# Performance work log

Measured on AMD Instinct MI355X. Metric: run time of the kernel, lower is better.

## Reference

```python
import jax, jax.numpy as jnp
import numpy as np

B, N, V, H, R, A, IN, K = 64, 512, 64, 512, 4, 18, 128, 32
EPS = 1e-8


def setup_inputs() -> dict:
    key = jax.random.key(0)
    ks = jax.random.split(key, 20)
    g = lambda i, shape, s=1.0: jax.random.normal(ks[i], shape, jnp.float32) * s
    u = lambda i, shape: jax.random.uniform(ks[i], shape, dtype=jnp.float32)
    cin = IN + R * V
    return dict(
        x=g(0, (B, IN)),
        h=g(1, (B, H), 0.1),
        c=g(2, (B, H), 0.1),
        memory=g(3, (B, N, V), 0.1),
        read_weights=u(4, (B, R, N)),
        write_weights=u(5, (B, N)),
        usage=u(6, (B, N)),
        link_matrix=u(7, (B, N, N)) * 0.01,
        precedence_weights=u(8, (B, N)),
        W_ih=g(9, (4 * H, cin), 0.05), W_hh=g(10, (4 * H, H), 0.05),
        b_ih=jnp.zeros(4 * H, jnp.float32), b_hh=jnp.zeros(4 * H, jnp.float32),
        W_read=g(11, (R, V + 4, H), 0.05), b_read=jnp.zeros((R, V + 4), jnp.float32),
        W_write=g(12, (3 * V + 3, H), 0.05), b_write=jnp.zeros(3 * V + 3, jnp.float32),
        W_pol=g(13, (A, H), 0.05), b_pol=jnp.zeros(A, jnp.float32),
        W_val=g(14, (1, H), 0.05), b_val=jnp.zeros(1, jnp.float32),
    )


def reference(x, h, c, memory, read_weights, write_weights, usage, link_matrix,
              precedence_weights, W_ih, W_hh, b_ih, b_hh, W_read, b_read,
              W_write, b_write, W_pol, b_pol, W_val, b_val):
    # ---- read heads (vectorized over R) ----
    ro = jnp.einsum('roh,bh->bro', W_read, h) + b_read            # [B,R,V+4]
    rkey = ro[..., :V]
    rbeta = jax.nn.softplus(ro[..., V])                           # [B,R]
    rpi = jax.nn.softmax(ro[..., V + 1:V + 4], axis=-1)           # backward/content/forward gates
    mem_norm = jnp.maximum(jnp.linalg.norm(memory, axis=-1), EPS)  # [B,N]
    key_norm = jnp.maximum(jnp.linalg.norm(rkey, axis=-1), EPS)    # [B,R]
    sim = jnp.einsum('bnv,brv->brn', memory, rkey) / (mem_norm[:, None, :] * key_norm[..., None])
    scores = rbeta[..., None] * sim                                # [B,R,N]
    kth = jax.lax.top_k(scores, K)[0][..., -1:]                    # sparse top-k mask
    cw = jax.nn.softmax(jnp.where(scores >= kth, scores, -jnp.inf), axis=-1)
    fw = jnp.einsum('bnm,brm->brn', link_matrix, read_weights)     # forward weighting L w
    bw = jnp.einsum('bmn,brm->brn', link_matrix, read_weights)     # backward weighting L^T w
    w_r = rpi[..., 0:1] * bw + rpi[..., 1:2] * cw + rpi[..., 2:3] * fw  # [B,R,N]
    rvec = jnp.einsum('brn,bnv->brv', w_r, memory).reshape(B, R * V)
    # ---- LSTM controller (torch LSTMCell gate order i,f,g,o) ----
    gates = jnp.concatenate([x, rvec], -1) @ W_ih.T + h @ W_hh.T + b_ih + b_hh
    i_g, f_g, g_g, o_g = jnp.split(gates, 4, axis=-1)
    c_new = jax.nn.sigmoid(f_g) * c + jax.nn.sigmoid(i_g) * jnp.tanh(g_g)
    h_new = jax.nn.sigmoid(o_g) * jnp.tanh(c_new)
    # ---- write head ----
    wo = h_new @ W_write.T + b_write                               # [B,3V+3]
    wkey = wo[:, :V]
    erase = jax.nn.sigmoid(wo[:, V:2 * V])
    add = jnp.tanh(wo[:, 2 * V:3 * V])
    wbeta = jax.nn.softplus(wo[:, 3 * V])
    g_a = jax.nn.sigmoid(wo[:, 3 * V + 1])
    g_w = jax.nn.sigmoid(wo[:, 3 * V + 2])
    wkey_norm = jnp.maximum(jnp.linalg.norm(wkey, axis=-1), EPS)
    wsim = jnp.einsum('bnv,bv->bn', memory, wkey) / (mem_norm * wkey_norm[:, None])
    cw_w = jax.nn.softmax(wbeta[:, None] * wsim, axis=-1)
    # allocation weighting from sorted usage (DNC Eq. 1)
    idx = jnp.argsort(usage, axis=-1)
    u_sorted = jnp.take_along_axis(usage, idx, -1)
    prod_prev = jnp.concatenate([jnp.ones((B, 1), usage.dtype), jnp.cumprod(u_sorted, -1)[:, :-1]], -1)
    a_sorted = (1.0 - u_sorted) * prod_prev
    alloc = jnp.take_along_axis(a_sorted, jnp.argsort(idx, -1), -1)
    write_w = g_w[:, None] * (g_a[:, None] * alloc + (1.0 - g_a)[:, None] * cw_w)  # [B,N]
    # ---- memory erase/add ----
    mem_new = memory * (1.0 - write_w[:, :, None] * erase[:, None, :]) + write_w[:, :, None] * add[:, None, :]
    # ---- usage (psi detached as in torch.no_grad) ----
    psi = jax.lax.stop_gradient(jnp.prod(1.0 - w_r, axis=1))
    usage_new = (usage + write_weights - usage * write_weights) * psi
    # ---- link matrix + precedence ----
    ws = jnp.sum(write_w, -1, keepdims=True)
    prec_new = (1.0 - ws) * precedence_weights + write_w
    decay = (1.0 - write_w[:, :, None]) * (1.0 - write_w[:, None, :])
    link_new = decay * link_matrix + write_w[:, :, None] * precedence_weights[:, None, :]
    link_new = link_new * (1.0 - jnp.eye(N, dtype=link_new.dtype))
    # ---- actor/critic heads ----
    logits = h_new @ W_pol.T + b_pol
    value = h_new @ W_val.T + b_val
    return (logits, value, h_new, c_new, mem_new, w_r, write_w, usage_new, link_new, prec_new)
```

## Files before the change

kernel.cpp:

```cpp
#include <hip/hip_runtime.h>
#include <math.h>

constexpr int Bb = 64, Nn = 512, Vv = 64, Hh = 512, Rr = 4, Aa = 18, INp = 128, KTOP = 32;
constexpr int CIN = 384;
constexpr int WOUT = 195;
#define EPSf 1e-8f

__device__ __forceinline__ float sigmoidf(float x){ return 1.f/(1.f+expf(-x)); }
__device__ __forceinline__ float softplusf(float x){ return (x>20.f)? x : log1pf(expf(x)); }
__device__ __forceinline__ float wave_reduce(float v){
  #pragma unroll
  for(int o=32;o>0;o>>=1) v += __shfl_down(v, o, 64);
  return v;
}
__device__ __forceinline__ unsigned f2ord(float f){
  unsigned u = __float_as_uint(f);
  return (u & 0x80000000u) ? ~u : (u | 0x80000000u);
}
__device__ __forceinline__ const float* wrow_sel(int d, const float* Ww, const float* Wp, const float* Wv){
  return (d < WOUT) ? Ww + (size_t)d*Hh : ((d < WOUT+Aa) ? Wp + (size_t)(d-WOUT)*Hh : Wv);
}

__global__ void k_stage1(const float* __restrict__ link, const float* __restrict__ rw,
                         const float* __restrict__ Wr, const float* __restrict__ brd,
                         const float* __restrict__ h, const float* __restrict__ mem,
                         float* __restrict__ fw, float* __restrict__ bwpart,
                         float* __restrict__ rvec, float* __restrict__ rp,
                         float* __restrict__ cw) {
  __shared__ __align__(16) float smem[6208];
  if (blockIdx.x < 512) {
    float* lds   = smem;
    float* ldsrw = smem + 4160;
    int b  = blockIdx.x >> 3;
    int st = blockIdx.x & 7;
    int tid = threadIdx.x;
    {
      const float4* rw4 = (const float4*)(rw + b*Rr*Nn);
      float4* lrw4 = (float4*)ldsrw;
      lrw4[tid] = rw4[tid];
      lrw4[tid+256] = rw4[tid+256];
    }
    if (blockIdx.x < 64) rvec[blockIdx.x*256 + tid] = 0.f;
    __syncthreads();
    int row = tid & 63, rr = tid >> 6;
    float facc = 0.f;
    const float4* lb4 = (const float4*)(link + (size_t)b*Nn*Nn);
    const float* rwn = ldsrw + rr*512 + st*64;
    for (int jt = 0; jt < 8; ++jt) {
      #pragma unroll
      for (int q = 0; q < 4; ++q) {
        int idx4 = tid*4 + q;
        int tr = idx4 >> 4;
        int c4 = idx4 & 15;
        float4 v = lb4[(size_t)(st*64 + tr)*128 + jt*16 + c4];
        int base = tr*65 + c4*4;
        lds[base] = v.x; lds[base+1] = v.y; lds[base+2] = v.z; lds[base+3] = v.w;
      }
      __syncthreads();
      const float* rwj = ldsrw + rr*512 + jt*64;
      float a = 0.f;
      #pragma unroll 8
      for (int j = 0; j < 64; ++j) a += lds[row*65 + j] * rwj[j];
      facc += a;
      float bacc = 0.f;
      #pragma unroll 8
      for (int n = 0; n < 64; ++n) bacc += lds[n*65 + row] * rwn[n];
      bwpart[((size_t)(st*Bb + b)*Rr + rr)*Nn + jt*64 + row] = bacc;
      __syncthreads();
    }
    fw[(b*Rr + rr)*Nn + st*64 + row] = facc;
  } else {
    float* sh  = smem;
    float* sro = smem + 512;
    unsigned long long* sk = (unsigned long long*)(smem + 592);
    float* sred = smem + 1616;
    float* skv  = smem + 1620;
    int blk = blockIdx.x - 512;
    int b = blk >> 2, r = blk & 3;
    int tid = threadIdx.x;
    int wv = tid >> 6, lane = tid & 63;
    const float* hb = h + b*Hh;
    for (int i = tid; i < 512; i += 256) sh[i] = hb[i];
    __syncthreads();
    const float* wbase = Wr + (size_t)(r*68)*Hh;
    int pbase = wv*17;
    #pragma unroll
    for (int g = 0; g < 4; ++g) {
      int p = pbase + g*4;
      const float *w0 = wbase + (size_t)p*Hh, *w1 = w0 + Hh, *w2 = w1 + Hh, *w3 = w2 + Hh;
      float a0=0,a1=0,a2=0,a3=0;
      #pragma unroll
      for (int t = 0; t < 8; ++t) {
        int k = lane + 64*t; float hv = sh[k];
        a0 += w0[k]*hv; a1 += w1[k]*hv; a2 += w2[k]*hv; a3 += w3[k]*hv;
      }
      #pragma unroll
      for (int o = 32; o > 0; o >>= 1) {
        a0 += __shfl_down(a0,o,64); a1 += __shfl_down(a1,o,64);
        a2 += __shfl_down(a2,o,64); a3 += __shfl_down(a3,o,64);
      }
      if (lane == 0) {
        sro[p]   = a0 + brd[r*68+p];   sro[p+1] = a1 + brd[r*68+p+1];
        sro[p+2] = a2 + brd[r*68+p+2]; sro[p+3] = a3 + brd[r*68+p+3];
      }
    }
    {
      int p = pbase + 16;
      const float* w0 = wbase + (size_t)p*Hh;
      float a0 = 0.f;
      #pragma unroll
      for (int t = 0; t < 8; ++t) { int k = lane + 64*t; a0 += w0[k]*sh[k]; }
      a0 = wave_reduce(a0);
      if (lane == 0) sro[p] = a0 + brd[r*68+p];
    }
    __syncthreads();
    if (wv == 0) {
      float kv = sro[lane];
      float k2 = wave_reduce(kv*kv);
      if (lane == 0) {
        float rbeta = softplusf(sro[64]);
        float sc = rbeta / fmaxf(sqrtf(k2), EPSf);
        float e0 = sro[65], e1 = sro[66], e2 = sro[67];
        float mm = fmaxf(e0, fmaxf(e1, e2));
        float x0 = expf(e0-mm), x1 = expf(e1-mm), x2 = expf(e2-mm);
        float inv = 1.f/(x0+x1+x2);
        float* rpb = rp + (b*4 + r)*4;
        rpb[0] = sc; rpb[1] = x0*inv; rpb[2] = x1*inv; rpb[3] = x2*inv;
        sro[68] = sc;
      }
    }
    __syncthreads();
    float sc = sro[68];
    const float4* key4 = (const float4*)sro;
    float v0, v1;
    {
      const float4* m4 = (const float4*)(mem + ((size_t)(b*Nn + tid))*Vv);
      float dot=0.f, nrm=0.f;
      #pragma unroll
      for (int i = 0; i < 16; ++i) {
        float4 mv = m4[i]; float4 kk = key4[i];
        dot += mv.x*kk.x + mv.y*kk.y + mv.z*kk.z + mv.w*kk.w;
        nrm += mv.x*mv.x + mv.y*mv.y + mv.z*mv.z + mv.w*mv.w;
      }
      v0 = sc * dot / fmaxf(sqrtf(nrm), EPSf);
    }
    {
      const float4* m4 = (const float4*)(mem + ((size_t)(b*Nn + tid + 256))*Vv);
      float dot=0.f, nrm=0.f;
      #pragma unroll
      for (int i = 0; i < 16; ++i) {
        float4 mv = m4[i]; float4 kk = key4[i];
        dot += mv.x*kk.x + mv.y*kk.y + mv.z*kk.z + mv.w*kk.w;
        nrm += mv.x*mv.x + mv.y*mv.y + mv.z*mv.z + mv.w*mv.w;
      }
      v1 = sc * dot / fmaxf(sqrtf(nrm), EPSf);
    }
    unsigned long long k0 = ((unsigned long long)f2ord(v0) << 32) | (unsigned)(511 - tid);
    unsigned long long k1 = ((unsigned long long)f2ord(v1) << 32) | (unsigned)(255 - tid);
    sk[tid] = k0; sk[tid+256] = k1;
    __syncthreads();
    int c0 = 0, c1 = 0;
    #pragma unroll 8
    for (int j = 0; j < 512; ++j) {
      unsigned long long kj = sk[j];
      c0 += (kj > k0); c1 += (kj > k1);
    }
    if (c0 == KTOP-1) skv[0] = v0;
    if (c1 == KTOP-1) skv[0] = v1;
    if (c0 == 0) skv[1] = v0;
    if (c1 == 0) skv[1] = v1;
    __syncthreads();
    float kth = skv[0], mx = skv[1];
    float e0 = (v0 >= kth) ? expf(v0-mx) : 0.f;
    float e1 = (v1 >= kth) ? expf(v1-mx) : 0.f;
    float s = wave_reduce(e0+e1);
    if (lane == 0) sred[wv] = s;
    __syncthreads();
    float inv = 1.f/(sred[0]+sred[1]+sred[2]+sred[3]);
    int brr = b*4 + r;
    cw[brr*Nn+tid]     = e0*inv;
    cw[brr*Nn+tid+256] = e1*inv;
  }
}

__global__ void k_wrrv(const float* __restrict__ bwpart, const float* __restrict__ cw,
                       const float* __restrict__ fw, const float* __restrict__ rp,
                       const float* __restrict__ usage, const float* __restrict__ wwt,
                       const float* __restrict__ mem,
                       float* __restrict__ out_wr, float* __restrict__ out_usage,
                       float* __restrict__ rvec) {
  __shared__ float swr[4][64];
  int b = blockIdx.x >> 3, ch = blockIdx.x & 7;
  int tid = threadIdx.x;
  int r = tid >> 6, nl = tid & 63;
  int n = ch*64 + nl;
  int brr = b*4 + r;
  float bwv = 0.f;
  #pragma unroll
  for (int chh = 0; chh < 8; ++chh)
    bwv += bwpart[((size_t)(chh*Bb + b)*Rr + r)*Nn + n];
  const float* rpb = rp + brr*4;
  float w = rpb[1]*bwv + rpb[2]*cw[brr*Nn+n] + rpb[3]*fw[brr*Nn+n];
  out_wr[brr*Nn+n] = w;
  swr[r][nl] = w;
  __syncthreads();
  if (tid < 64) {
    int idx = b*Nn + ch*64 + tid;
    float psi = (1.f-swr[0][tid])*(1.f-swr[1][tid])*(1.f-swr[2][tid])*(1.f-swr[3][tid]);
    float u = usage[idx], wt = wwt[idx];
    out_usage[idx] = (u + wt - u*wt) * psi;
  }
  const float* mb = mem + ((size_t)b*Nn + ch*64)*Vv + nl;
  float acc = 0.f;
  #pragma unroll 16
  for (int t = 0; t < 64; ++t) acc += swr[r][t] * mb[t*Vv];
  atomicAdd(&rvec[brr*Vv + nl], acc);
}

__global__ void k_gates_lstm(const float* __restrict__ x, const float* __restrict__ rvec,
                             const float* __restrict__ h, const float* __restrict__ Wih,
                             const float* __restrict__ Whh, const float* __restrict__ bih,
                             const float* __restrict__ bhh, const float* __restrict__ c,
                             float* __restrict__ out_h, float* __restrict__ out_c) {
  int gid = blockIdx.x*4 + (threadIdx.x>>6);
  int lane = threadIdx.x & 63;
  int hh = gid >> 4;
  int bt = gid & 15;
  float acc[4][4] = {};
  #pragma unroll
  for (int t = 0; t < 6; ++t) {
    int k = lane + 64*t;
    float u[4], w[4];
    #pragma unroll
    for (int i = 0; i < 4; ++i) {
      int b = bt*4 + i;
      u[i] = (k < INp) ? x[b*INp + k] : rvec[b*(Rr*Vv) + k - INp];
      w[i] = Wih[(size_t)(i*Hh + hh)*CIN + k];
    }
    #pragma unroll
    for (int g = 0; g < 4; ++g)
      #pragma unroll
      for (int bb = 0; bb < 4; ++bb) acc[g][bb] += w[g]*u[bb];
  }
  #pragma unroll
  for (int t = 0; t < 8; ++t) {
    int k = lane + 64*t;
    float u[4], w[4];
    #pragma unroll
    for (int i = 0; i < 4; ++i) {
      u[i] = h[(bt*4+i)*Hh + k];
      w[i] = Whh[(size_t)(i*Hh + hh)*Hh + k];
    }
    #pragma unroll
    for (int g = 0; g < 4; ++g)
      #pragma unroll
      for (int bb = 0; bb < 4; ++bb) acc[g][bb] += w[g]*u[bb];
  }
  #pragma unroll
  for (int g = 0; g < 4; ++g)
    #pragma unroll
    for (int bb = 0; bb < 4; ++bb) acc[g][bb] = wave_reduce(acc[g][bb]);
  if (lane == 0) {
    float bsum[4];
    #pragma unroll
    for (int g = 0; g < 4; ++g) bsum[g] = bih[g*Hh + hh] + bhh[g*Hh + hh];
    #pragma unroll
    for (int bb = 0; bb < 4; ++bb) {
      int b = bt*4 + bb;
      float ig = sigmoidf(acc[0][bb] + bsum[0]);
      float fg = sigmoidf(acc[1][bb] + bsum[1]);
      float gg = tanhf   (acc[2][bb] + bsum[2]);
      float og = sigmoidf(acc[3][bb] + bsum[3]);
      float cn = fg * c[b*Hh + hh] + ig * gg;
      float hn = og * tanhf(cn);
      out_c[b*Hh + hh] = cn;
      out_h[b*Hh + hh] = hn;
    }
  }
}

__global__ void k_tail(const float* __restrict__ hn, const float* __restrict__ Ww,
                       const float* __restrict__ bw_, const float* __restrict__ Wp,
                       const float* __restrict__ bp, const float* __restrict__ Wv,
                       const float* __restrict__ bv, const float* __restrict__ usage,
                       const float* __restrict__ prec, const float* __restrict__ mem,
                       float* __restrict__ wo, float* __restrict__ out_logits,
                       float* __restrict__ out_value, float* __restrict__ out_ww,
                       float* __restrict__ out_prec) {
  __shared__ __align__(16) float sh[512];
  __shared__ __align__(16) float swo[200];
  __shared__ unsigned long long sk[512];
  __shared__ float su[512];
  __shared__ float cp[512];
  __shared__ float sred[8];
  int b = blockIdx.x, tid = threadIdx.x;
  int wv = tid >> 6, lane = tid & 63;
  const float* hb = hn + b*Hh;
  sh[tid] = hb[tid]; sh[tid+256] = hb[tid+256];
  __syncthreads();
  const float4* sh4 = (const float4*)sh;
  float4 h0 = sh4[lane*2], h1 = sh4[lane*2+1];
  int dbeg = wv*54, dend = (dbeg + 54 < 214) ? dbeg + 54 : 214;
  for (int p = dbeg; p < dend; p += 4) {
    int d1 = (p+1 < 213) ? p+1 : 213, d2 = (p+2 < 213) ? p+2 : 213, d3 = (p+3 < 213) ? p+3 : 213;
    const float4* w04 = (const float4*)wrow_sel(p,  Ww, Wp, Wv);
    const float4* w14 = (const float4*)wrow_sel(d1, Ww, Wp, Wv);
    const float4* w24 = (const float4*)wrow_sel(d2, Ww, Wp, Wv);
    const float4* w34 = (const float4*)wrow_sel(d3, Ww, Wp, Wv);
    float4 A0 = w04[lane*2], B0 = w04[lane*2+1];
    float4 A1 = w14[lane*2], B1 = w14[lane*2+1];
    float4 A2 = w24[lane*2], B2 = w24[lane*2+1];
    float4 A3 = w34[lane*2], B3 = w34[lane*2+1];
    float a0 = A0.x*h0.x + A0.y*h0.y + A0.z*h0.z + A0.w*h0.w
             + B0.x*h1.x + B0.y*h1.y + B0.z*h1.z + B0.w*h1.w;
    float a1 = A1.x*h0.x + A1.y*h0.y + A1.z*h0.z + A1.w*h0.w
             + B1.x*h1.x + B1.y*h1.y + B1.z*h1.z + B1.w*h1.w;
    float a2 = A2.x*h0.x + A2.y*h0.y + A2.z*h0.z + A2.w*h0.w
             + B2.x*h1.x + B2.y*h1.y + B2.z*h1.z + B2.w*h1.w;
    float a3 = A3.x*h0.x + A3.y*h0.y + A3.z*h0.z + A3.w*h0.w
             + B3.x*h1.x + B3.y*h1.y + B3.z*h1.z + B3.w*h1.w;
    #pragma unroll
    for (int o = 32; o > 0; o >>= 1) {
      a0 += __shfl_down(a0,o,64); a1 += __shfl_down(a1,o,64);
      a2 += __shfl_down(a2,o,64); a3 += __shfl_down(a3,o,64);
    }
    if (lane == 0) {
      float av[4] = {a0,a1,a2,a3};
      #pragma unroll
      for (int i = 0; i < 4; ++i) {
        int d = p + i;
        if (d >= dend) break;
        float a = av[i];
        if (d < WOUT)          { float vv = a + bw_[d]; swo[d] = vv; wo[b*WOUT+d] = vv; }
        else if (d < WOUT+Aa)  { out_logits[b*Aa + (d-WOUT)] = a + bp[d-WOUT]; }
        else                   { out_value[b] = a + bv[0]; }
      }
    }
  }
  __syncthreads();
  float wbeta = softplusf(swo[192]);
  const float4* key4 = (const float4*)swo;
  float s0, s1;
  {
    const float4* m4 = (const float4*)(mem + ((size_t)(b*Nn + tid))*Vv);
    float dot=0.f, nrm=0.f, kn=0.f;
    #pragma unroll
    for (int i = 0; i < 16; ++i) {
      float4 mv = m4[i]; float4 kk = key4[i];
      dot += mv.x*kk.x + mv.y*kk.y + mv.z*kk.z + mv.w*kk.w;
      nrm += mv.x*mv.x + mv.y*mv.y + mv.z*mv.z + mv.w*mv.w;
      kn  += kk.x*kk.x + kk.y*kk.y + kk.z*kk.z + kk.w*kk.w;
    }
    s0 = wbeta * dot / (fmaxf(sqrtf(nrm), EPSf) * fmaxf(sqrtf(kn), EPSf));
  }
  {
    const float4* m4 = (const float4*)(mem + ((size_t)(b*Nn + tid + 256))*Vv);
    float dot=0.f, nrm=0.f, kn=0.f;
    #pragma unroll
    for (int i = 0; i < 16; ++i) {
      float4 mv = m4[i]; float4 kk = key4[i];
      dot += mv.x*kk.x + mv.y*kk.y + mv.z*kk.z + mv.w*kk.w;
      nrm += mv.x*mv.x + mv.y*mv.y + mv.z*mv.z + mv.w*mv.w;
      kn  += kk.x*kk.x + kk.y*kk.y + kk.z*kk.z + kk.w*kk.w;
    }
    s1 = wbeta * dot / (fmaxf(sqrtf(nrm), EPSf) * fmaxf(sqrtf(kn), EPSf));
  }
  float u0 = usage[b*Nn+tid], u1 = usage[b*Nn+tid+256];
  unsigned long long k0 = ((unsigned long long)f2ord(u0) << 32) | (unsigned)tid;
  unsigned long long k1 = ((unsigned long long)f2ord(u1) << 32) | (unsigned)(tid+256);
  sk[tid] = k0; sk[tid+256] = k1;
  float mxl = fmaxf(s0, s1);
  #pragma unroll
  for (int o = 32; o > 0; o >>= 1) mxl = fmaxf(mxl, __shfl_down(mxl,o,64));
  if (lane == 0) sred[wv] = mxl;
  __syncthreads();
  float mx = fmaxf(fmaxf(sred[0],sred[1]), fmaxf(sred[2],sred[3]));
  float e0 = expf(s0-mx), e1 = expf(s1-mx);
  float ssum = wave_reduce(e0+e1);
  if (lane == 0) sred[4+wv] = ssum;
  int r0 = 0, r1 = 0;
  #pragma unroll 8
  for (int j = 0; j < 512; ++j) {
    unsigned long long kj = sk[j];
    r0 += (kj < k0); r1 += (kj < k1);
  }
  __syncthreads();
  float cinv = 1.f/(sred[4]+sred[5]+sred[6]+sred[7]);
  float c0 = e0*cinv, c1 = e1*cinv;
  su[r0] = u0; su[r1] = u1;
  __syncthreads();
  cp[tid] = su[tid]; cp[tid+256] = su[tid+256];
  __syncthreads();
  for (int d = 1; d < 512; d <<= 1) {
    float t0 = cp[tid]     * ((tid >= d)     ? cp[tid-d]     : 1.f);
    float t1 = cp[tid+256] * ((tid+256 >= d) ? cp[tid+256-d] : 1.f);
    __syncthreads();
    cp[tid] = t0; cp[tid+256] = t1;
    __syncthreads();
  }
  float pp0 = (r0 == 0) ? 1.f : cp[r0-1];
  float pp1 = (r1 == 0) ? 1.f : cp[r1-1];
  float a0 = (1.f-u0)*pp0, a1 = (1.f-u1)*pp1;
  float ga = sigmoidf(swo[193]);
  float gw = sigmoidf(swo[194]);
  float wv0 = gw * (ga*a0 + (1.f-ga)*c0);
  float wv1 = gw * (ga*a1 + (1.f-ga)*c1);
  out_ww[b*Nn+tid]     = wv0;
  out_ww[b*Nn+tid+256] = wv1;
  float ws_ = wave_reduce(wv0+wv1);
  if (lane == 0) sred[wv] = ws_;
  __syncthreads();
  float wsum = sred[0]+sred[1]+sred[2]+sred[3];
  out_prec[b*Nn+tid]     = (1.f-wsum)*prec[b*Nn+tid]     + wv0;
  out_prec[b*Nn+tid+256] = (1.f-wsum)*prec[b*Nn+tid+256] + wv1;
}

__global__ void k_memlink(const float* __restrict__ link, const float* __restrict__ ww,
                          const float* __restrict__ prec, const float* __restrict__ mem,
                          const float* __restrict__ wo, float* __restrict__ out_link,
                          float* __restrict__ out_mem) {
  int bid = blockIdx.x;
  if (bid < 16384) {
    int idx4 = bid*256 + threadIdx.x;
    int base = idx4*4;
    int b = base >> 18;
    int rem = base & 262143;
    int i = rem >> 9;
    int j0 = rem & 511;
    float wi = ww[b*Nn + i];
    float fi = 1.f - wi;
    float4 lv = *(const float4*)(link + base);
    float4 wj = *(const float4*)(ww + b*Nn + j0);
    float4 pj = *(const float4*)(prec + b*Nn + j0);
    float4 o;
    o.x = fi*(1.f-wj.x)*lv.x + wi*pj.x;
    o.y = fi*(1.f-wj.y)*lv.y + wi*pj.y;
    o.z = fi*(1.f-wj.z)*lv.z + wi*pj.z;
    o.w = fi*(1.f-wj.w)*lv.w + wi*pj.w;
    if (i >= j0 && i < j0+4) {
      if (i == j0) o.x = 0.f;
      else if (i == j0+1) o.y = 0.f;
      else if (i == j0+2) o.z = 0.f;
      else o.w = 0.f;
    }
    *(float4*)(out_link + base) = o;
  } else {
    int idx4 = (bid - 16384)*256 + threadIdx.x;
    int base = idx4*4;
    int b = base >> 15;
    int rem = base & 32767;
    int n = rem >> 6;
    int v0 = rem & 63;
    float w = ww[b*Nn + n];
    const float* wob = wo + b*WOUT;
    float4 m = *(const float4*)(mem + base);
    float4 o;
    float e, a;
    e = sigmoidf(wob[64+v0+0]); a = tanhf(wob[128+v0+0]); o.x = m.x*(1.f-w*e)+w*a;
    e = sigmoidf(wob[64+v0+1]); a = tanhf(wob[128+v0+1]); o.y = m.y*(1.f-w*e)+w*a;
    e = sigmoidf(wob[64+v0+2]); a = tanhf(wob[128+v0+2]); o.z = m.z*(1.f-w*e)+w*a;
    e = sigmoidf(wob[64+v0+3]); a = tanhf(wob[128+v0+3]); o.w = m.w*(1.f-w*e)+w*a;
    *(float4*)(out_mem + base) = o;
  }
}

extern "C" void kernel_launch(void* const* d_in, const int* in_sizes, int n_in,
                              void* d_out, int out_size, void* d_ws, size_t ws_size,
                              hipStream_t stream) {
  const float* x    = (const float*)d_in[0];
  const float* h    = (const float*)d_in[1];
  const float* c    = (const float*)d_in[2];
  const float* mem  = (const float*)d_in[3];
  const float* rw   = (const float*)d_in[4];
  const float* wwt  = (const float*)d_in[5];
  const float* usage= (const float*)d_in[6];
  const float* link = (const float*)d_in[7];
  const float* prec = (const float*)d_in[8];
  const float* Wih  = (const float*)d_in[9];
  const float* Whh  = (const float*)d_in[10];
  const float* bih  = (const float*)d_in[11];
  const float* bhh  = (const float*)d_in[12];
  const float* Wr   = (const float*)d_in[13];
  const float* br   = (const float*)d_in[14];
  const float* Ww   = (const float*)d_in[15];
  const float* bw_  = (const float*)d_in[16];
  const float* Wp   = (const float*)d_in[17];
  const float* bp   = (const float*)d_in[18];
  const float* Wv   = (const float*)d_in[19];
  const float* bv   = (const float*)d_in[20];

  float* out = (float*)d_out;
  float* o_logits = out + 0;
  float* o_value  = out + 1152;
  float* o_h      = out + 1216;
  float* o_c      = out + 33984;
  float* o_mem    = out + 66752;
  float* o_wr     = out + 2163904;
  float* o_ww     = out + 2294976;
  float* o_usage  = out + 2327744;
  float* o_link   = out + 2360512;
  float* o_prec   = out + 19137728;

  float* ws = (float*)d_ws;
  float* ws_rp     = ws;
  float* ws_cw     = ws + 1024;
  float* ws_fw     = ws + 132096;
  float* ws_bwpart = ws + 263168;
  float* ws_rvec   = ws + 1311744;
  float* ws_wo     = ws + 1328128;

  k_stage1     <<<dim3(768),        dim3(256), 0, stream>>>(link, rw, Wr, br, h, mem, ws_fw, ws_bwpart, ws_rvec, ws_rp, ws_cw);
  k_wrrv       <<<dim3(Bb*8),       dim3(256), 0, stream>>>(ws_bwpart, ws_cw, ws_fw, ws_rp, usage, wwt, mem, o_wr, o_usage, ws_rvec);
  k_gates_lstm <<<dim3(2048),       dim3(256), 0, stream>>>(x, ws_rvec, h, Wih, Whh, bih, bhh, c, o_h, o_c);
  k_tail       <<<dim3(Bb),         dim3(256), 0, stream>>>(o_h, Ww, bw_, Wp, bp, Wv, bv, usage, prec, mem, ws_wo, o_logits, o_value, o_ww, o_prec);
  k_memlink    <<<dim3(16384+2048), dim3(256), 0, stream>>>(link, o_ww, prec, mem, ws_wo, o_link, o_mem);
}
```

Baseline: 292.5 us.

## Restructure link matvec in stage1 with prefetch and specialized forward/backward waves

The forward and backward link-matrix products in k_stage1 now use 128-row slabs per block, halving the link-processing block count. The next 64-column tile is prefetched into registers while the current tile is computed, so global loads overlap compute. Half of each block's waves compute the forward product for all four read heads at once from a transposed read-weight array; the other half compute the backward partials with float4 column accumulation. The cost is fewer resident blocks, higher register pressure (a 64-float per-thread array plus the prefetch buffers), and barriers placed inside wave-divergent branches.

After: 430.2 us. 47.1% more time.

```diff
diff --git a/kernel.cpp b/kernel.cpp
--- a/kernel.cpp
+++ b/kernel.cpp
@@ -27,55 +27,106 @@
                          float* __restrict__ fw, float* __restrict__ bwpart,
                          float* __restrict__ rvec, float* __restrict__ rp,
                          float* __restrict__ cw) {
-  __shared__ __align__(16) float smem[6208];
-  if (blockIdx.x < 512) {
-    float* lds   = smem;
-    float* ldsrw = smem + 4160;
-    int b  = blockIdx.x >> 3;
-    int st = blockIdx.x & 7;
+  __shared__ __align__(16) float4 smem4[2688];
+  if (blockIdx.x < 256) {
+    float4* tile4 = smem4;
+    float4* rwT4  = smem4 + 2176;
+    float*  rwT   = (float*)rwT4;
+    int b  = blockIdx.x >> 2;
+    int st = blockIdx.x & 3;
     int tid = threadIdx.x;
+    if (blockIdx.x < 64) rvec[blockIdx.x*256 + tid] = 0.f;
     {
-      const float4* rw4 = (const float4*)(rw + b*Rr*Nn);
-      float4* lrw4 = (float4*)ldsrw;
-      lrw4[tid] = rw4[tid];
-      lrw4[tid+256] = rw4[tid+256];
-    }
-    if (blockIdx.x < 64) rvec[blockIdx.x*256 + tid] = 0.f;
-    __syncthreads();
-    int row = tid & 63, rr = tid >> 6;
-    float facc = 0.f;
+      const float4* rw4g = (const float4*)(rw + b*Rr*Nn);
+      #pragma unroll
+      for (int q = 0; q < 2; ++q) {
+        int f = tid + 256*q;
+        float4 v = rw4g[f];
+        int r = f >> 7, n4 = f & 127;
+        rwT[(4*n4+0)*4 + r] = v.x; rwT[(4*n4+1)*4 + r] = v.y;
+        rwT[(4*n4+2)*4 + r] = v.z; rwT[(4*n4+3)*4 + r] = v.w;
+      }
+    }
     const float4* lb4 = (const float4*)(link + (size_t)b*Nn*Nn);
-    const float* rwn = ldsrw + rr*512 + st*64;
-    for (int jt = 0; jt < 8; ++jt) {
-      #pragma unroll
-      for (int q = 0; q < 4; ++q) {
-        int idx4 = tid*4 + q;
-        int tr = idx4 >> 4;
-        int c4 = idx4 & 15;
-        float4 v = lb4[(size_t)(st*64 + tr)*128 + jt*16 + c4];
-        int base = tr*65 + c4*4;
-        lds[base] = v.x; lds[base+1] = v.y; lds[base+2] = v.z; lds[base+3] = v.w;
-      }
-      __syncthreads();
-      const float* rwj = ldsrw + rr*512 + jt*64;
-      float a = 0.f;
-      #pragma unroll 8
-      for (int j = 0; j < 64; ++j) a += lds[row*65 + j] * rwj[j];
-      facc += a;
-      float bacc = 0.f;
-      #pragma unroll 8
-      for (int n = 0; n < 64; ++n) bacc += lds[n*65 + row] * rwn[n];
-      bwpart[((size_t)(st*Bb + b)*Rr + rr)*Nn + jt*64 + row] = bacc;
-      __syncthreads();
-    }
-    fw[(b*Rr + rr)*Nn + st*64 + row] = facc;
+    float4 pf[8];
+    int prow[8], pc4[8];
+    #pragma unroll
+    for (int q = 0; q < 8; ++q) {
+      int f = tid + 256*q;
+      prow[q] = f >> 4; pc4[q] = f & 15;
+      pf[q] = lb4[(size_t)(st*128 + prow[q])*128 + pc4[q]];
+    }
+    #pragma unroll
+    for (int q = 0; q < 8; ++q) tile4[prow[q]*17 + pc4[q]] = pf[q];
+    __syncthreads();
+    if (tid < 128) {
+      int row = tid;
+      float facc[4] = {0.f,0.f,0.f,0.f};
+      for (int jt = 0; jt < 8; ++jt) {
+        if (jt < 7) {
+          #pragma unroll
+          for (int q = 0; q < 8; ++q)
+            pf[q] = lb4[(size_t)(st*128 + prow[q])*128 + (jt+1)*16 + pc4[q]];
+        }
+        #pragma unroll
+        for (int j4 = 0; j4 < 16; ++j4) {
+          float4 t = tile4[row*17 + j4];
+          float4 w0 = rwT4[jt*64 + 4*j4 + 0];
+          float4 w1 = rwT4[jt*64 + 4*j4 + 1];
+          float4 w2 = rwT4[jt*64 + 4*j4 + 2];
+          float4 w3 = rwT4[jt*64 + 4*j4 + 3];
+          facc[0] += t.x*w0.x + t.y*w1.x + t.z*w2.x + t.w*w3.x;
+          facc[1] += t.x*w0.y + t.y*w1.y + t.z*w2.y + t.w*w3.y;
+          facc[2] += t.x*w0.z + t.y*w1.z + t.z*w2.z + t.w*w3.z;
+          facc[3] += t.x*w0.w + t.y*w1.w + t.z*w2.w + t.w*w3.w;
+        }
+        __syncthreads();
+        if (jt < 7) {
+          #pragma unroll
+          for (int q = 0; q < 8; ++q) tile4[prow[q]*17 + pc4[q]] = pf[q];
+          __syncthreads();
+        }
+      }
+      #pragma unroll
+      for (int r = 0; r < 4; ++r)
+        fw[(b*Rr + r)*Nn + st*128 + row] = facc[r];
+    } else {
+      int idx = tid - 128;
+      int col4 = idx & 15, r = (idx>>4) & 3, half = idx >> 6;
+      float rwn[64];
+      #pragma unroll
+      for (int g = 0; g < 64; ++g) rwn[g] = rwT[(st*128 + half*64 + g)*4 + r];
+      for (int jt = 0; jt < 8; ++jt) {
+        if (jt < 7) {
+          #pragma unroll
+          for (int q = 0; q < 8; ++q)
+            pf[q] = lb4[(size_t)(st*128 + prow[q])*128 + (jt+1)*16 + pc4[q]];
+        }
+        float4 bacc = make_float4(0.f,0.f,0.f,0.f);
+        #pragma unroll
+        for (int n = 0; n < 64; ++n) {
+          float4 t = tile4[(half*64 + n)*17 + col4];
+          float s = rwn[n];
+          bacc.x += t.x*s; bacc.y += t.y*s; bacc.z += t.z*s; bacc.w += t.w*s;
+        }
+        int chunk = st*2 + half;
+        *(float4*)(bwpart + ((size_t)(chunk*Bb + b)*Rr + r)*Nn + jt*64 + col4*4) = bacc;
+        __syncthreads();
+        if (jt < 7) {
+          #pragma unroll
+          for (int q = 0; q < 8; ++q) tile4[prow[q]*17 + pc4[q]] = pf[q];
+          __syncthreads();
+        }
+      }
+    }
   } else {
+    float* smem = (float*)smem4;
     float* sh  = smem;
     float* sro = smem + 512;
     unsigned long long* sk = (unsigned long long*)(smem + 592);
     float* sred = smem + 1616;
     float* skv  = smem + 1620;
-    int blk = blockIdx.x - 512;
+    int blk = blockIdx.x - 256;
     int b = blk >> 2, r = blk & 3;
     int tid = threadIdx.x;
     int wv = tid >> 6, lane = tid & 63;
@@ -509,7 +560,7 @@
   float* ws_rvec   = ws + 1311744;
   float* ws_wo     = ws + 1328128;
 
-  k_stage1     <<<dim3(768),        dim3(256), 0, stream>>>(link, rw, Wr, br, h, mem, ws_fw, ws_bwpart, ws_rvec, ws_rp, ws_cw);
+  k_stage1     <<<dim3(512),        dim3(256), 0, stream>>>(link, rw, Wr, br, h, mem, ws_fw, ws_bwpart, ws_rvec, ws_rp, ws_cw);
   k_wrrv       <<<dim3(Bb*8),       dim3(256), 0, stream>>>(ws_bwpart, ws_cw, ws_fw, ws_rp, usage, wwt, mem, o_wr, o_usage, ws_rvec);
   k_gates_lstm <<<dim3(2048),       dim3(256), 0, stream>>>(x, ws_rvec, h, Wih, Whh, bih, bhh, c, o_h, o_c);
   k_tail       <<<dim3(Bb),         dim3(256), 0, stream>>>(o_h, Ww, bw_, Wp, bp, Wv, bv, usage, prec, mem, ws_wo, o_logits, o_value, o_ww, o_prec);
```

## Compute link forward/backward products from registers with wave reductions instead of LDS tiles

Applied to the files above, without the earlier changes.

The link-matrix pass in stage 1 no longer stages 64x64 tiles through LDS with two barriers per tile. Each wave now streams whole rows of the link matrix straight into registers with coalesced loads, keeps the read weights in registers, and computes the forward product with wave shuffle reductions. The backward product is accumulated per column in registers and combined across waves through LDS at the end. This removes most LDS traffic and barriers, at the cost of many more registers per thread (which may lower occupancy) and more shuffle work.

Result: slower. 311.7 us (+6.6%).

```diff
diff --git a/kernel.cpp b/kernel.cpp
--- a/kernel.cpp
+++ b/kernel.cpp
@@ -27,48 +27,69 @@
                          float* __restrict__ fw, float* __restrict__ bwpart,
                          float* __restrict__ rvec, float* __restrict__ rp,
                          float* __restrict__ cw) {
-  __shared__ __align__(16) float smem[6208];
+  __shared__ __align__(16) float smem[8192];
   if (blockIdx.x < 512) {
-    float* lds   = smem;
-    float* ldsrw = smem + 4160;
+    float (*bl)[4][512] = reinterpret_cast<float (*)[4][512]>(smem);
+    if (blockIdx.x < 64) rvec[blockIdx.x*256 + threadIdx.x] = 0.f;
     int b  = blockIdx.x >> 3;
-    int st = blockIdx.x & 7;
+    int ch = blockIdx.x & 7;
+    int wv = threadIdx.x >> 6, lane = threadIdx.x & 63;
+    const float* rwb = rw + b*Rr*Nn;
+    float rwv[4][8];
+    #pragma unroll
+    for (int r = 0; r < 4; ++r)
+      #pragma unroll
+      for (int t = 0; t < 8; ++t) rwv[r][t] = rwb[r*512 + lane + 64*t];
+    float bwacc[8][4] = {};
+    const float* lb = link + (size_t)b*Nn*Nn;
+    int n0 = ch*64 + wv*16;
+    for (int i = 0; i < 16; i += 2) {
+      int na = n0 + i, nb = n0 + i + 1;
+      float lka[8], lkb[8];
+      #pragma unroll
+      for (int t = 0; t < 8; ++t) lka[t] = lb[na*512 + lane + 64*t];
+      #pragma unroll
+      for (int t = 0; t < 8; ++t) lkb[t] = lb[nb*512 + lane + 64*t];
+      float sa0 = rwb[na], sa1 = rwb[512+na], sa2 = rwb[1024+na], sa3 = rwb[1536+na];
+      float sb0 = rwb[nb], sb1 = rwb[512+nb], sb2 = rwb[1024+nb], sb3 = rwb[1536+nb];
+      float fa0=0,fa1=0,fa2=0,fa3=0, fb0=0,fb1=0,fb2=0,fb3=0;
+      #pragma unroll
+      for (int t = 0; t < 8; ++t) {
+        float va = lka[t], vb = lkb[t];
+        fa0 += va*rwv[0][t]; fa1 += va*rwv[1][t]; fa2 += va*rwv[2][t]; fa3 += va*rwv[3][t];
+        fb0 += vb*rwv[0][t]; fb1 += vb*rwv[1][t]; fb2 += vb*rwv[2][t]; fb3 += vb*rwv[3][t];
+        bwacc[t][0] += va*sa0 + vb*sb0;
+        bwacc[t][1] += va*sa1 + vb*sb1;
+        bwacc[t][2] += va*sa2 + vb*sb2;
+        bwacc[t][3] += va*sa3 + vb*sb3;
+      }
+      #pragma unroll
+      for (int o = 32; o > 0; o >>= 1) {
+        fa0 += __shfl_down(fa0,o,64); fa1 += __shfl_down(fa1,o,64);
+        fa2 += __shfl_down(fa2,o,64); fa3 += __shfl_down(fa3,o,64);
+        fb0 += __shfl_down(fb0,o,64); fb1 += __shfl_down(fb1,o,64);
+        fb2 += __shfl_down(fb2,o,64); fb3 += __shfl_down(fb3,o,64);
+      }
+      if (lane == 0) {
+        fw[(b*Rr+0)*Nn+na] = fa0; fw[(b*Rr+1)*Nn+na] = fa1;
+        fw[(b*Rr+2)*Nn+na] = fa2; fw[(b*Rr+3)*Nn+na] = fa3;
+        fw[(b*Rr+0)*Nn+nb] = fb0; fw[(b*Rr+1)*Nn+nb] = fb1;
+        fw[(b*Rr+2)*Nn+nb] = fb2; fw[(b*Rr+3)*Nn+nb] = fb3;
+      }
+    }
+    #pragma unroll
+    for (int t = 0; t < 8; ++t)
+      #pragma unroll
+      for (int r = 0; r < 4; ++r) bl[wv][r][lane + 64*t] = bwacc[t][r];
+    __syncthreads();
     int tid = threadIdx.x;
-    {
-      const float4* rw4 = (const float4*)(rw + b*Rr*Nn);
-      float4* lrw4 = (float4*)ldsrw;
-      lrw4[tid] = rw4[tid];
-      lrw4[tid+256] = rw4[tid+256];
-    }
-    if (blockIdx.x < 64) rvec[blockIdx.x*256 + tid] = 0.f;
-    __syncthreads();
-    int row = tid & 63, rr = tid >> 6;
-    float facc = 0.f;
-    const float4* lb4 = (const float4*)(link + (size_t)b*Nn*Nn);
-    const float* rwn = ldsrw + rr*512 + st*64;
-    for (int jt = 0; jt < 8; ++jt) {
-      #pragma unroll
-      for (int q = 0; q < 4; ++q) {
-        int idx4 = tid*4 + q;
-        int tr = idx4 >> 4;
-        int c4 = idx4 & 15;
-        float4 v = lb4[(size_t)(st*64 + tr)*128 + jt*16 + c4];
-        int base = tr*65 + c4*4;
-        lds[base] = v.x; lds[base+1] = v.y; lds[base+2] = v.z; lds[base+3] = v.w;
-      }
-      __syncthreads();
-      const float* rwj = ldsrw + rr*512 + jt*64;
-      float a = 0.f;
-      #pragma unroll 8
-      for (int j = 0; j < 64; ++j) a += lds[row*65 + j] * rwj[j];
-      facc += a;
-      float bacc = 0.f;
-      #pragma unroll 8
-      for (int n = 0; n < 64; ++n) bacc += lds[n*65 + row] * rwn[n];
-      bwpart[((size_t)(st*Bb + b)*Rr + rr)*Nn + jt*64 + row] = bacc;
-      __syncthreads();
-    }
-    fw[(b*Rr + rr)*Nn + st*64 + row] = facc;
+    #pragma unroll
+    for (int q = 0; q < 8; ++q) {
+      int idx = q*256 + tid;
+      int r = idx >> 9, j = idx & 511;
+      float v = bl[0][r][j] + bl[1][r][j] + bl[2][r][j] + bl[3][r][j];
+      bwpart[((size_t)(ch*Bb + b)*Rr + r)*Nn + j] = v;
+    }
   } else {
     float* sh  = smem;
     float* sro = smem + 512;
```
